# Kernel optimization log

Hardware: AMD Instinct MI355X
Metric: run time of the kernel (lower is better)

The kernel has to match this reference:

```python
import jax, jax.numpy as jnp
import numpy as np


def setup_inputs() -> dict:
    key = jax.random.key(0)
    k1, k2, k3 = jax.random.split(key, 3)
    D, N, K = 512, 131072, 64
    x = jax.random.normal(k1, (D, N), dtype=jnp.float32)
    a_bar = jax.random.uniform(k2, (K, N), dtype=jnp.float32)
    c = jax.random.normal(k3, (K, D), dtype=jnp.float32)
    return {"x": x, "a_bar": a_bar, "c": c}


def reference(x, a_bar, c):
    # V[k, d] = sum_n a_bar[k, n] * (x[d, n] - c[k, d])
    #         = (a_bar @ x.T)[k, d] - c[k, d] * sum_n a_bar[k, n]
    # Fused form: one GEMM + one row-sum, never materializing (K, D, N) residuals.
    ax = jnp.einsum('kn,dn->kd', a_bar, x)        # (K, D)
    a_sum = jnp.sum(a_bar, axis=1, keepdims=True)  # (K, 1)
    V = ax - c * a_sum                              # (K, D)
    return V
```

## Files before the change

### kernel.cpp

```cpp
#include <hip/hip_runtime.h>
#include <hip/hip_bf16.h>


#define K_ROWS 64
#define D_COLS 512
#define N_RED  131072LL
#define TOTAL_STEPS 4096
#define XBY 8192
#define ABY 4096
#define BUFB (XBY + ABY)

typedef __attribute__((ext_vector_type(8))) short short8;
typedef __attribute__((ext_vector_type(4))) float f32x4;

static __device__ __forceinline__ short f2bf(float f) {
    __bf16 h = (__bf16)f;
    return __builtin_bit_cast(short, h);
}
static __device__ __forceinline__ float bf2f(unsigned short u) {
    return __builtin_bit_cast(float, (unsigned)u << 16);
}
static __device__ __forceinline__ short8 cvt8(float4 a, float4 b) {
    short8 r;
    r[0] = f2bf(a.x); r[1] = f2bf(a.y); r[2] = f2bf(a.z); r[3] = f2bf(a.w);
    r[4] = f2bf(b.x); r[5] = f2bf(b.y); r[6] = f2bf(b.z); r[7] = f2bf(b.w);
    return r;
}

__global__ __launch_bounds__(512, 6) void vlad_stage1(
    const float* __restrict__ x, const float* __restrict__ ab,
    unsigned short* __restrict__ pax, float* __restrict__ pasum, int S)
{
    __shared__ __align__(16) char smem[2][BUFB];

    const int bid = blockIdx.x;
    const int x7  = bid & 7;
    const int g   = (bid >> 3) & 3;
    const int m   = bid >> 5;
    const int s   = m * 8 + x7;
    const int tid = threadIdx.x;
    const int w   = tid >> 6, l = tid & 63, lr = l & 15, lg = l >> 4;
    const int d0  = g * 128;

    const int st0 = (int)(((long long)s       * TOTAL_STEPS) / S);
    const int st1 = (int)(((long long)(s + 1) * TOTAL_STEPS) / S);

    const int xrow = tid >> 2, xslot = tid & 3;
    const int xoff = xrow * 64 + ((xslot ^ ((xrow >> 1) & 3)) << 4);
    const float* gx = x + (size_t)(d0 + xrow) * N_RED + xslot * 8;

    const int aoff = ABY ? (XBY + xrow * 64 + ((xslot ^ ((xrow >> 1) & 3)) << 4)) : 0;
    const float* ga = ab + (size_t)xrow * N_RED + xslot * 8;
    const bool at = (tid < 256);

    const int swz = (lr >> 1) & 3;
    const int fxo = (w * 16 + lr) * 64 + ((lg ^ swz) << 4);
    int fao[4];
    #pragma unroll
    for (int t = 0; t < 4; ++t)
        fao[t] = XBY + (t * 16 + lr) * 64 + ((lg ^ swz) << 4);

    f32x4 acc[4] = {};
    float asum = 0.f;
    float4 L0, L1, L2, L3;

    auto issue = [&](int it) {
        const float* p = gx + (size_t)it * 32;
        L0 = *(const float4*)(p);
        L1 = *(const float4*)(p + 4);
        if (at) {
            const float* q = ga + (size_t)it * 32;
            L2 = *(const float4*)(q);
            L3 = *(const float4*)(q + 4);
        }
    };
    auto commit = [&](char* buf) {
        *(short8*)(buf + xoff) = cvt8(L0, L1);
        if (at) {
            *(short8*)(buf + aoff) = cvt8(L2, L3);
            float ssum = ((L2.x + L2.y) + (L2.z + L2.w))
                       + ((L3.x + L3.y) + (L3.z + L3.w));
            ssum += __shfl_xor(ssum, 1, 64);
            ssum += __shfl_xor(ssum, 2, 64);
            asum += ssum;
        }
    };

    issue(st0);
    commit(smem[0]);

    int cur = 0;
    #pragma unroll 1
    for (int it = st0; it < st1; ++it) {
        const bool more = (it + 1 < st1);
        __syncthreads();
        if (more) issue(it + 1);

        const char* b = smem[cur];
        short8 xf  = *(const short8*)(b + fxo);
        short8 a0f = *(const short8*)(b + fao[0]);
        short8 a1f = *(const short8*)(b + fao[1]);
        short8 a2f = *(const short8*)(b + fao[2]);
        short8 a3f = *(const short8*)(b + fao[3]);
        acc[0] = __builtin_amdgcn_mfma_f32_16x16x32_bf16(a0f, xf, acc[0], 0, 0, 0);
        acc[1] = __builtin_amdgcn_mfma_f32_16x16x32_bf16(a1f, xf, acc[1], 0, 0, 0);
        acc[2] = __builtin_amdgcn_mfma_f32_16x16x32_bf16(a2f, xf, acc[2], 0, 0, 0);
        acc[3] = __builtin_amdgcn_mfma_f32_16x16x32_bf16(a3f, xf, acc[3], 0, 0, 0);

        if (more) commit(smem[cur ^ 1]);
        cur ^= 1;
    }

    unsigned short* dst = pax + (size_t)s * (K_ROWS * D_COLS);
    #pragma unroll
    for (int t = 0; t < 4; ++t)
        #pragma unroll
        for (int r = 0; r < 4; ++r)
            dst[(((g * 8 + w) * 4 + t) * 4 + r) * 64 + l] =
                (unsigned short)f2bf(acc[t][r]);

    if (g == 0 && at && (tid & 3) == 0)
        pasum[s * K_ROWS + (tid >> 2)] = asum;
}

__global__ __launch_bounds__(256) void vlad_stage2(
    const unsigned short* __restrict__ pax, const float* __restrict__ pasum,
    const float* __restrict__ c, float* __restrict__ out, int S)
{
    __shared__ float red[256];
    __shared__ float ared[256];
    const int t  = threadIdx.x;
    const int fo = t & 63;
    const int sp = t >> 6;
    const int fb = blockIdx.x * 64;
    const int f  = fb + fo;

    float acc = 0.f;
    for (int s = sp; s < S; s += 4)
        acc += bf2f(pax[(size_t)s * (K_ROWS * D_COLS) + f]);
    red[t] = acc;

    const int R = (fb >> 6) & 3, T = (fb >> 8) & 3;
    const int ka = T * 16 + (t & 3) * 4 + R;
    float pa = 0.f;
    for (int s2 = t >> 2; s2 < S; s2 += 64)
        pa += pasum[s2 * K_ROWS + ka];
    ared[t] = pa;
    __syncthreads();

    for (int st = 128; st >= 4; st >>= 1) {
        if (t < st) ared[t] += ared[t + st];
        __syncthreads();
    }
    if (sp == 0) {
        const int lr = f & 15, lg = (f >> 4) & 3;
        const int r  = (f >> 6) & 3, tt = (f >> 8) & 3;
        const int w  = (f >> 10) & 7, gg = (f >> 13) & 3;
        const int k  = tt * 16 + lg * 4 + r;
        const int d  = gg * 128 + w * 16 + lr;
        float v = red[t] + red[t + 64] + red[t + 128] + red[t + 192];
        out[k * D_COLS + d] = v - c[k * D_COLS + d] * ared[lg];
    }
}

extern "C" void kernel_launch(void* const* d_in, const int* in_sizes, int n_in,
                              void* d_out, int out_size, void* d_ws, size_t ws_size,
                              hipStream_t stream)
{
    const float* x  = (const float*)d_in[0];
    const float* ab = (const float*)d_in[1];
    const float* c  = (const float*)d_in[2];
    float* out = (float*)d_out;

    int S = 192;
    while (S > 24 &&
           (size_t)S * ((size_t)K_ROWS * D_COLS * 2 + K_ROWS * 4) > ws_size)
        S >>= 1;

    unsigned short* pax = (unsigned short*)d_ws;
    float* pasum = (float*)((char*)d_ws + (size_t)S * K_ROWS * D_COLS * 2);

    vlad_stage1<<<dim3(4 * S), dim3(512), 0, stream>>>(x, ab, pax, pasum, S);
    vlad_stage2<<<dim3((K_ROWS * D_COLS) / 64), dim3(256), 0, stream>>>(pax, pasum, c, out, S);
}
```

Before: 71.80 us.

## Double the per-step K chunk to 64 and rebalance loads across all threads

Each main-loop iteration now stages 64 reduction elements instead of 32, so the number of barriers per block and the loop overhead are halved, and each sync is followed by two MFMA k-slices. The a_bar load is spread over all 512 threads (8 per row) rather than half, removing the thread-divergent branch. The per-step shuffle reduction of the a_bar row sum is replaced by a single shuffle reduction at the end. LDS per block doubles to 48KB for the two buffers, which may lower occupancy below the launch-bounds target of 6 blocks per CU.

```diff
diff --git a/kernel.cpp b/kernel.cpp
--- a/kernel.cpp
+++ b/kernel.cpp
@@ -5,9 +5,9 @@
 #define K_ROWS 64
 #define D_COLS 512
 #define N_RED  131072LL
-#define TOTAL_STEPS 4096
-#define XBY 8192
-#define ABY 4096
+#define TOTAL_STEPS 2048
+#define XBY 16384
+#define ABY 8192
 #define BUFB (XBY + ABY)
 
 typedef __attribute__((ext_vector_type(8))) short short8;
@@ -45,45 +45,44 @@
     const int st0 = (int)(((long long)s       * TOTAL_STEPS) / S);
     const int st1 = (int)(((long long)(s + 1) * TOTAL_STEPS) / S);
 
-    const int xrow = tid >> 2, xslot = tid & 3;
-    const int xoff = xrow * 64 + ((xslot ^ ((xrow >> 1) & 3)) << 4);
-    const float* gx = x + (size_t)(d0 + xrow) * N_RED + xslot * 8;
+    const int xrow = tid >> 2, xq = tid & 3;
+    const float* gx = x + (size_t)(d0 + xrow) * N_RED + xq * 16;
+    const int xo0 = xrow * 128 + (((xq * 2)     ^ (xrow & 7)) << 4);
+    const int xo1 = xrow * 128 + (((xq * 2 + 1) ^ (xrow & 7)) << 4);
+    const int arow = tid >> 3, aq = tid & 7;
+    const float* ga = ab + (size_t)arow * N_RED + aq * 8;
+    const int ao0 = XBY + arow * 128 + ((aq ^ (arow & 7)) << 4);
 
-    const int aoff = ABY ? (XBY + xrow * 64 + ((xslot ^ ((xrow >> 1) & 3)) << 4)) : 0;
-    const float* ga = ab + (size_t)xrow * N_RED + xslot * 8;
-    const bool at = (tid < 256);
-
-    const int swz = (lr >> 1) & 3;
-    const int fxo = (w * 16 + lr) * 64 + ((lg ^ swz) << 4);
-    int fao[4];
+    const int swz = lr & 7;
+    int fx[2], fa[4][2];
     #pragma unroll
-    for (int t = 0; t < 4; ++t)
-        fao[t] = XBY + (t * 16 + lr) * 64 + ((lg ^ swz) << 4);
+    for (int kk = 0; kk < 2; ++kk) {
+        fx[kk] = (w * 16 + lr) * 128 + ((((kk << 2) | lg) ^ swz) << 4);
+        #pragma unroll
+        for (int t = 0; t < 4; ++t)
+            fa[t][kk] = XBY + (t * 16 + lr) * 128 + ((((kk << 2) | lg) ^ swz) << 4);
+    }
 
     f32x4 acc[4] = {};
     float asum = 0.f;
-    float4 L0, L1, L2, L3;
+    float4 X0, X1, X2, X3, A0, A1;
 
     auto issue = [&](int it) {
-        const float* p = gx + (size_t)it * 32;
-        L0 = *(const float4*)(p);
-        L1 = *(const float4*)(p + 4);
-        if (at) {
-            const float* q = ga + (size_t)it * 32;
-            L2 = *(const float4*)(q);
-            L3 = *(const float4*)(q + 4);
-        }
+        const float* p = gx + (size_t)it * 64;
+        X0 = *(const float4*)(p);
+        X1 = *(const float4*)(p + 4);
+        X2 = *(const float4*)(p + 8);
+        X3 = *(const float4*)(p + 12);
+        const float* q = ga + (size_t)it * 64;
+        A0 = *(const float4*)(q);
+        A1 = *(const float4*)(q + 4);
     };
     auto commit = [&](char* buf) {
-        *(short8*)(buf + xoff) = cvt8(L0, L1);
-        if (at) {
-            *(short8*)(buf + aoff) = cvt8(L2, L3);
-            float ssum = ((L2.x + L2.y) + (L2.z + L2.w))
-                       + ((L3.x + L3.y) + (L3.z + L3.w));
-            ssum += __shfl_xor(ssum, 1, 64);
-            ssum += __shfl_xor(ssum, 2, 64);
-            asum += ssum;
-        }
+        *(short8*)(buf + xo0) = cvt8(X0, X1);
+        *(short8*)(buf + xo1) = cvt8(X2, X3);
+        *(short8*)(buf + ao0) = cvt8(A0, A1);
+        asum += ((A0.x + A0.y) + (A0.z + A0.w))
+              + ((A1.x + A1.y) + (A1.z + A1.w));
     };
 
     issue(st0);
@@ -97,15 +96,18 @@
         if (more) issue(it + 1);
 
         const char* b = smem[cur];
-        short8 xf  = *(const short8*)(b + fxo);
-        short8 a0f = *(const short8*)(b + fao[0]);
-        short8 a1f = *(const short8*)(b + fao[1]);
-        short8 a2f = *(const short8*)(b + fao[2]);
-        short8 a3f = *(const short8*)(b + fao[3]);
-        acc[0] = __builtin_amdgcn_mfma_f32_16x16x32_bf16(a0f, xf, acc[0], 0, 0, 0);
-        acc[1] = __builtin_amdgcn_mfma_f32_16x16x32_bf16(a1f, xf, acc[1], 0, 0, 0);
-        acc[2] = __builtin_amdgcn_mfma_f32_16x16x32_bf16(a2f, xf, acc[2], 0, 0, 0);
-        acc[3] = __builtin_amdgcn_mfma_f32_16x16x32_bf16(a3f, xf, acc[3], 0, 0, 0);
+        #pragma unroll
+        for (int kk = 0; kk < 2; ++kk) {
+            short8 xf  = *(const short8*)(b + fx[kk]);
+            short8 a0f = *(const short8*)(b + fa[0][kk]);
+            short8 a1f = *(const short8*)(b + fa[1][kk]);
+            short8 a2f = *(const short8*)(b + fa[2][kk]);
+            short8 a3f = *(const short8*)(b + fa[3][kk]);
+            acc[0] = __builtin_amdgcn_mfma_f32_16x16x32_bf16(a0f, xf, acc[0], 0, 0, 0);
+            acc[1] = __builtin_amdgcn_mfma_f32_16x16x32_bf16(a1f, xf, acc[1], 0, 0, 0);
+            acc[2] = __builtin_amdgcn_mfma_f32_16x16x32_bf16(a2f, xf, acc[2], 0, 0, 0);
+            acc[3] = __builtin_amdgcn_mfma_f32_16x16x32_bf16(a3f, xf, acc[3], 0, 0, 0);
+        }
 
         if (more) commit(smem[cur ^ 1]);
         cur ^= 1;
@@ -119,8 +121,12 @@
             dst[(((g * 8 + w) * 4 + t) * 4 + r) * 64 + l] =
                 (unsigned short)f2bf(acc[t][r]);
 
-    if (g == 0 && at && (tid & 3) == 0)
-        pasum[s * K_ROWS + (tid >> 2)] = asum;
+    if (g == 0) {
+        asum += __shfl_xor(asum, 1, 64);
+        asum += __shfl_xor(asum, 2, 64);
+        asum += __shfl_xor(asum, 4, 64);
+        if ((tid & 7) == 0) pasum[s * K_ROWS + arow] = asum;
+    }
 }
 
 __global__ __launch_bounds__(256) void vlad_stage2(
```

Result: slower. 83.88 us (+16.8%).

## Load x fragments directly to registers and triple-buffer a_bar in LDS

Applied to the files above, without the earlier changes.

Each lane now loads its own x fragment from global memory straight into registers in MFMA layout and converts it to bf16 in place, so x no longer goes through shared memory. Only a_bar is staged in LDS, using a 3-deep ring with a two-step register prefetch, and the per-step shuffle reduction of the a_bar row sums is moved to the end of the kernel. This cuts LDS traffic and footprint and removes per-step shuffles. The cost is more live registers and a global x access pattern that may coalesce less well.

```diff
diff --git a/kernel.cpp b/kernel.cpp
--- a/kernel.cpp
+++ b/kernel.cpp
@@ -6,9 +6,7 @@
 #define D_COLS 512
 #define N_RED  131072LL
 #define TOTAL_STEPS 4096
-#define XBY 8192
-#define ABY 4096
-#define BUFB (XBY + ABY)
+#define ABUF 4096
 
 typedef __attribute__((ext_vector_type(8))) short short8;
 typedef __attribute__((ext_vector_type(4))) float f32x4;
@@ -31,7 +29,7 @@
     const float* __restrict__ x, const float* __restrict__ ab,
     unsigned short* __restrict__ pax, float* __restrict__ pasum, int S)
 {
-    __shared__ __align__(16) char smem[2][BUFB];
+    __shared__ __align__(16) char smem[3][ABUF];
 
     const int bid = blockIdx.x;
     const int x7  = bid & 7;
@@ -45,70 +43,62 @@
     const int st0 = (int)(((long long)s       * TOTAL_STEPS) / S);
     const int st1 = (int)(((long long)(s + 1) * TOTAL_STEPS) / S);
 
-    const int xrow = tid >> 2, xslot = tid & 3;
-    const int xoff = xrow * 64 + ((xslot ^ ((xrow >> 1) & 3)) << 4);
-    const float* gx = x + (size_t)(d0 + xrow) * N_RED + xslot * 8;
+    const float* gx = x + (size_t)(d0 + w * 16 + lr) * N_RED + lg * 8;
 
-    const int aoff = ABY ? (XBY + xrow * 64 + ((xslot ^ ((xrow >> 1) & 3)) << 4)) : 0;
-    const float* ga = ab + (size_t)xrow * N_RED + xslot * 8;
-    const bool at = (tid < 256);
+    const bool at  = (tid < 256);
+    const int arow = tid >> 2, aq = tid & 3;
+    const float* ga = ab + (size_t)arow * N_RED + aq * 8;
+    const int awoff = arow * 64 + ((aq ^ (arow & 3)) << 4);
 
-    const int swz = (lr >> 1) & 3;
-    const int fxo = (w * 16 + lr) * 64 + ((lg ^ swz) << 4);
-    int fao[4];
+    const int swz = lr & 3;
+    int fa[4];
     #pragma unroll
     for (int t = 0; t < 4; ++t)
-        fao[t] = XBY + (t * 16 + lr) * 64 + ((lg ^ swz) << 4);
+        fa[t] = (t * 16 + lr) * 64 + ((lg ^ swz) << 4);
 
     f32x4 acc[4] = {};
     float asum = 0.f;
-    float4 L0, L1, L2, L3;
+    float4 X0, X1, A0, A1, B0, B1;
 
-    auto issue = [&](int it) {
-        const float* p = gx + (size_t)it * 32;
-        L0 = *(const float4*)(p);
-        L1 = *(const float4*)(p + 4);
-        if (at) {
-            const float* q = ga + (size_t)it * 32;
-            L2 = *(const float4*)(q);
-            L3 = *(const float4*)(q + 4);
-        }
-    };
-    auto commit = [&](char* buf) {
-        *(short8*)(buf + xoff) = cvt8(L0, L1);
-        if (at) {
-            *(short8*)(buf + aoff) = cvt8(L2, L3);
-            float ssum = ((L2.x + L2.y) + (L2.z + L2.w))
-                       + ((L3.x + L3.y) + (L3.z + L3.w));
-            ssum += __shfl_xor(ssum, 1, 64);
-            ssum += __shfl_xor(ssum, 2, 64);
-            asum += ssum;
-        }
-    };
+    if (at) { const float* q = ga + (size_t)st0 * 32; A0 = *(const float4*)q; A1 = *(const float4*)(q + 4); }
+    { const float* p = gx + (size_t)st0 * 32; X0 = *(const float4*)p; X1 = *(const float4*)(p + 4); }
+    if (at) {
+        *(short8*)(smem[0] + awoff) = cvt8(A0, A1);
+        asum += ((A0.x + A0.y) + (A0.z + A0.w)) + ((A1.x + A1.y) + (A1.z + A1.w));
+    }
+    if (at && st0 + 1 < st1) { const float* q = ga + (size_t)(st0 + 1) * 32; A0 = *(const float4*)q; A1 = *(const float4*)(q + 4); }
 
-    issue(st0);
-    commit(smem[0]);
-
-    int cur = 0;
+    int rb = 0;
     #pragma unroll 1
     for (int it = st0; it < st1; ++it) {
-        const bool more = (it + 1 < st1);
         __syncthreads();
-        if (more) issue(it + 1);
+        if (at && it + 2 < st1) {
+            const float* q = ga + (size_t)(it + 2) * 32;
+            B0 = *(const float4*)q; B1 = *(const float4*)(q + 4);
+        }
+        short8 xf = cvt8(X0, X1);
+        if (it + 1 < st1) {
+            const float* p = gx + (size_t)(it + 1) * 32;
+            X0 = *(const float4*)p; X1 = *(const float4*)(p + 4);
+        }
 
-        const char* b = smem[cur];
-        short8 xf  = *(const short8*)(b + fxo);
-        short8 a0f = *(const short8*)(b + fao[0]);
-        short8 a1f = *(const short8*)(b + fao[1]);
-        short8 a2f = *(const short8*)(b + fao[2]);
-        short8 a3f = *(const short8*)(b + fao[3]);
+        const char* b = smem[rb];
+        short8 a0f = *(const short8*)(b + fa[0]);
+        short8 a1f = *(const short8*)(b + fa[1]);
+        short8 a2f = *(const short8*)(b + fa[2]);
+        short8 a3f = *(const short8*)(b + fa[3]);
         acc[0] = __builtin_amdgcn_mfma_f32_16x16x32_bf16(a0f, xf, acc[0], 0, 0, 0);
         acc[1] = __builtin_amdgcn_mfma_f32_16x16x32_bf16(a1f, xf, acc[1], 0, 0, 0);
         acc[2] = __builtin_amdgcn_mfma_f32_16x16x32_bf16(a2f, xf, acc[2], 0, 0, 0);
         acc[3] = __builtin_amdgcn_mfma_f32_16x16x32_bf16(a3f, xf, acc[3], 0, 0, 0);
 
-        if (more) commit(smem[cur ^ 1]);
-        cur ^= 1;
+        if (at && it + 1 < st1) {
+            int wb_ = (rb + 1 == 3) ? 0 : rb + 1;
+            *(short8*)(smem[wb_] + awoff) = cvt8(A0, A1);
+            asum += ((A0.x + A0.y) + (A0.z + A0.w)) + ((A1.x + A1.y) + (A1.z + A1.w));
+            A0 = B0; A1 = B1;
+        }
+        rb = (rb + 1 == 3) ? 0 : rb + 1;
     }
 
     unsigned short* dst = pax + (size_t)s * (K_ROWS * D_COLS);
@@ -119,8 +109,11 @@
             dst[(((g * 8 + w) * 4 + t) * 4 + r) * 64 + l] =
                 (unsigned short)f2bf(acc[t][r]);
 
-    if (g == 0 && at && (tid & 3) == 0)
-        pasum[s * K_ROWS + (tid >> 2)] = asum;
+    if (g == 0 && at) {
+        asum += __shfl_xor(asum, 1, 64);
+        asum += __shfl_xor(asum, 2, 64);
+        if (aq == 0) pasum[s * K_ROWS + arow] = asum;
+    }
 }
 
 __global__ __launch_bounds__(256) void vlad_stage2(
```

Measured after the change: 74.03 us. 3.1% more time.
